# Performance work log

Hardware: AMD Instinct MI355X
Metric: run time of the kernel (lower is better)

The kernel has to match this reference:

```python
import jax, jax.numpy as jnp
import numpy as np
from math import sqrt

D_MODEL = 1024
N_HEADS = 16
D_KEYS = 64
D_LLM = 4096
B, L, N = 8, 512, 1000


def _init_params(key):
    ks = jax.random.split(key, 20)
    s = 0.02
    def lin(k, din, dout):
        return jax.random.normal(k, (din, dout), jnp.float32) * s
    p = {}
    for i, pre in enumerate(('t', 'd')):
        o = i * 8
        p[pre + '_Wq'] = lin(ks[o + 0], D_MODEL, N_HEADS * D_KEYS)
        p[pre + '_bq'] = jnp.zeros((N_HEADS * D_KEYS,), jnp.float32)
        p[pre + '_Wk'] = lin(ks[o + 1], D_LLM, N_HEADS * D_KEYS)
        p[pre + '_bk'] = jnp.zeros((N_HEADS * D_KEYS,), jnp.float32)
        p[pre + '_Wv'] = lin(ks[o + 2], D_LLM, N_HEADS * D_KEYS)
        p[pre + '_bv'] = jnp.zeros((N_HEADS * D_KEYS,), jnp.float32)
        p[pre + '_Wo'] = lin(ks[o + 3], N_HEADS * D_KEYS, D_LLM)
        p[pre + '_bo'] = jnp.zeros((D_LLM,), jnp.float32)
    # adaptive fusion gate MLP: Linear(2d->d), ReLU, Linear(d->1), Sigmoid
    p['g_W1'] = jax.random.normal(ks[16], (2 * D_MODEL, D_MODEL), jnp.float32) * sqrt(2.0 / (2 * D_MODEL))
    p['g_b1'] = jnp.zeros((D_MODEL,), jnp.float32)
    p['g_W2'] = jax.random.normal(ks[17], (D_MODEL, 1), jnp.float32) * s
    p['g_b2'] = jnp.zeros((1,), jnp.float32)  # gate_bias_init = 0.0
    return p


def setup_inputs() -> dict:
    key = jax.random.key(0)
    k1, k2, k3, k4, kp = jax.random.split(key, 5)
    inp = {
        'trend_embedding': jax.random.normal(k1, (B, L, D_MODEL), jnp.float32),
        'detail_embedding': jax.random.normal(k2, (B, L, D_MODEL), jnp.float32),
        'trend_prototypes': jax.random.normal(k3, (N, D_LLM), jnp.float32),
        'detail_prototypes': jax.random.normal(k4, (N, D_LLM), jnp.float32),
    }
    inp.update(_init_params(kp))
    return inp


def _reprogram(x, protos, Wq, bq, Wk, bk, Wv, bv, Wo, bo):
    # x: (B,L,d_model), protos: (S,d_llm)
    b, l, _ = x.shape
    s = protos.shape[0]
    q = (x @ Wq + bq).reshape(b, l, N_HEADS, D_KEYS)
    k = (protos @ Wk + bk).reshape(s, N_HEADS, D_KEYS)
    v = (protos @ Wv + bv).reshape(s, N_HEADS, D_KEYS)
    scale = 1.0 / sqrt(D_KEYS)
    scores = jnp.einsum('blhe,she->bhls', q, k)  # (B,H,L,S)
    A = jax.nn.softmax(scale * scores, axis=-1)  # dropout is eval-mode identity
    out = jnp.einsum('bhls,she->blhe', A, v).reshape(b, l, N_HEADS * D_KEYS)
    return out @ Wo + bo  # (B,L,d_llm)


def reference(trend_embedding, detail_embedding, trend_prototypes, detail_prototypes,
              t_Wq, t_bq, t_Wk, t_bk, t_Wv, t_bv, t_Wo, t_bo,
              d_Wq, d_bq, d_Wk, d_bk, d_Wv, d_bv, d_Wo, d_bo,
              g_W1, g_b1, g_W2, g_b2):
    sem_trend = _reprogram(trend_embedding, trend_prototypes,
                           t_Wq, t_bq, t_Wk, t_bk, t_Wv, t_bv, t_Wo, t_bo)
    sem_detail = _reprogram(detail_embedding, detail_prototypes,
                            d_Wq, d_bq, d_Wk, d_bk, d_Wv, d_bv, d_Wo, d_bo)
    # adaptive gate from raw embeddings
    combined = jnp.concatenate([trend_embedding, detail_embedding], axis=-1)
    h = jax.nn.relu(combined @ g_W1 + g_b1)
    gate = jax.nn.sigmoid(h @ g_W2 + g_b2)  # (B,L,1)
    return gate * sem_trend + (1.0 - gate) * sem_detail
```

## Files before the change

kernel.cpp:

```cpp
#include <hip/hip_runtime.h>

typedef unsigned short u16;
typedef unsigned int u32;
typedef __attribute__((ext_vector_type(4))) u16 u16x4;
typedef __attribute__((ext_vector_type(8))) u16 u16x8;
typedef __attribute__((ext_vector_type(4))) float f32x4;
typedef __attribute__((ext_vector_type(8))) __bf16 bf16x8;

#define DEV static __device__ __forceinline__

DEV u16 f2bf(float f) {
    u32 u = __builtin_bit_cast(u32, f);
    return (u16)((u + 0x7FFFu + ((u >> 16) & 1u)) >> 16);
}
DEV float bf2f(u16 h) { return __builtin_bit_cast(float, (u32)h << 16); }

DEV f32x4 mfma16(u16x8 a, u16x8 b, f32x4 c) {
    return __builtin_amdgcn_mfma_f32_16x16x32_bf16(
        __builtin_bit_cast(bf16x8, a), __builtin_bit_cast(bf16x8, b), c, 0, 0, 0);
}

DEV void gload16(const void* g, void* l) {
    __builtin_amdgcn_global_load_lds(
        (const __attribute__((address_space(1))) void*)g,
        (__attribute__((address_space(3))) void*)l, 16, 0, 0);
}


__global__ __launch_bounds__(256) void k_build_xcomb(
    const float* __restrict__ tr, const float* __restrict__ de, u16* __restrict__ out) {
    int i = blockIdx.x * 256 + threadIdx.x;
    int m = i >> 9;
    int c = (i & 511) * 4;
    const float* src = (c < 1024) ? (tr + (size_t)m * 1024 + c)
                                  : (de + (size_t)m * 1024 + (c - 1024));
    f32x4 v = *(const f32x4*)src;
    u16x4 o = { f2bf(v[0]), f2bf(v[1]), f2bf(v[2]), f2bf(v[3]) };
    *(u16x4*)(out + (size_t)m * 2048 + c) = o;
}

__global__ __launch_bounds__(256) void k_convert(
    const float* __restrict__ in, u16* __restrict__ out, int n4) {
    int i = blockIdx.x * 256 + threadIdx.x;
    if (i >= n4) return;
    f32x4 v = ((const f32x4*)in)[i];
    u16x4 o = { f2bf(v[0]), f2bf(v[1]), f2bf(v[2]), f2bf(v[3]) };
    ((u16x4*)out)[i] = o;
}


__global__ void k_transpose_f2b(const float* __restrict__ in, u16* __restrict__ out,
                                int R, int C, int ldo) {
    __shared__ float t[32][33];
    int c0 = blockIdx.x * 32, r0 = blockIdx.y * 32;
    int tx = threadIdx.x, ty = threadIdx.y;
#pragma unroll
    for (int j = 0; j < 4; j++)
        t[ty + j * 8][tx] = in[(size_t)(r0 + ty + j * 8) * C + c0 + tx];
    __syncthreads();
#pragma unroll
    for (int j = 0; j < 4; j++)
        out[(size_t)(c0 + ty + j * 8) * ldo + r0 + tx] = f2bf(t[tx][ty + j * 8]);
}

__global__ void k_transpose_b2b(const u16* __restrict__ in, int ldi,
                                u16* __restrict__ out, int ldo, int R, int C) {
    __shared__ u16 t[32][33];
    int c0 = blockIdx.x * 32, r0 = blockIdx.y * 32;
    int tx = threadIdx.x, ty = threadIdx.y;
#pragma unroll
    for (int j = 0; j < 4; j++)
        t[ty + j * 8][tx] = in[(size_t)(r0 + ty + j * 8) * ldi + c0 + tx];
    __syncthreads();
#pragma unroll
    for (int j = 0; j < 4; j++)
        out[(size_t)(c0 + ty + j * 8) * ldo + r0 + tx] = t[tx][ty + j * 8];
}

#define MODE_BF16 0
#define MODE_BF16_RELU 1
#define MODE_F32_GATED 2

__global__ __launch_bounds__(256) void k_gemm128(
    const u16* __restrict__ A0, const u16* __restrict__ A1, int lda,
    const u16* __restrict__ B0, const u16* __restrict__ B1, int K,
    void* __restrict__ o0, void* __restrict__ o1, int ldc, int mode,
    const float* __restrict__ b1_0, const float* __restrict__ b1_1,
    const float* __restrict__ b2_0, const float* __restrict__ b2_1,
    const float* __restrict__ gate) {
    __shared__ u16 As[128 * 32];
    __shared__ u16 Bs[128 * 32];
    const int z = blockIdx.z;
    const u16* A = z ? A1 : A0;
    const u16* Bt = z ? B1 : B0;
    void* outp = z ? o1 : o0;
    const float* bias1 = z ? b1_1 : b1_0;
    const float* bias2 = z ? b2_1 : b2_0;

    const int tid = threadIdx.x, lane = tid & 63, wid = tid >> 6;
    const int l16 = lane & 15, l4 = lane >> 4;
    const int n0 = blockIdx.x * 128, m0 = blockIdx.y * 128;
    const int wm = (wid >> 1) * 64, wn = (wid & 1) * 64;

    const int srow = wid * 32 + (lane >> 2);
    const int scol = (lane & 3) * 8;
    const u16* gA = A + (size_t)(m0 + srow) * lda + scol;
    const u16* gB = Bt + (size_t)(n0 + srow) * (size_t)K + scol;
    u16* lA = As + wid * 32 * 32;
    u16* lB = Bs + wid * 32 * 32;

    f32x4 acc[4][4] = {};

    for (int k0 = 0; k0 < K; k0 += 32) {
        gload16(gA, lA);
        gload16(gA + (size_t)16 * lda, lA + 16 * 32);
        gload16(gB, lB);
        gload16(gB + (size_t)16 * K, lB + 16 * 32);
        gA += 32;
        gB += 32;
        __syncthreads();
        u16x8 af[4], bfr[4];
#pragma unroll
        for (int m = 0; m < 4; m++) af[m] = *(const u16x8*)&As[(wm + m * 16 + l16) * 32 + l4 * 8];
#pragma unroll
        for (int n = 0; n < 4; n++) bfr[n] = *(const u16x8*)&Bs[(wn + n * 16 + l16) * 32 + l4 * 8];
#pragma unroll
        for (int m = 0; m < 4; m++)
#pragma unroll
            for (int n = 0; n < 4; n++)
                acc[m][n] = mfma16(af[m], bfr[n], acc[m][n]);
        __syncthreads();
    }

#pragma unroll
    for (int m = 0; m < 4; m++) {
#pragma unroll
        for (int n = 0; n < 4; n++) {
            int col = n0 + wn + n * 16 + l16;
#pragma unroll
            for (int j = 0; j < 4; j++) {
                int row = m0 + wm + m * 16 + l4 * 4 + j;
                float v = acc[m][n][j];
                if (mode == MODE_F32_GATED) {
                    float g = gate[row];
                    ((float*)outp)[(size_t)row * ldc + col] =
                        v + g * bias1[col] + (1.f - g) * bias2[col];
                } else {
                    float bb = (bias2 != nullptr && col >= 1024) ? bias2[col - 1024]
                                                                 : bias1[col];
                    v += bb;
                    if (mode == MODE_BF16_RELU) v = fmaxf(v, 0.f);
                    ((u16*)outp)[(size_t)row * ldc + col] = f2bf(v);
                }
            }
        }
    }
}

__global__ __launch_bounds__(256) void k_gate(const u16* __restrict__ h,
                                              const float* __restrict__ W2,
                                              const float* __restrict__ b2,
                                              float* __restrict__ gate) {
    int row = blockIdx.x * 4 + (threadIdx.x >> 6);
    int lane = threadIdx.x & 63;
    const u16* hp = h + (size_t)row * 1024 + lane * 16;
    u16x8 a = *(const u16x8*)hp;
    u16x8 b = *(const u16x8*)(hp + 8);
    const f32x4* wp = (const f32x4*)(W2 + lane * 16);
    f32x4 w0 = wp[0], w1 = wp[1], w2 = wp[2], w3 = wp[3];
    float s = 0.f;
#pragma unroll
    for (int i = 0; i < 4; i++) {
        s += bf2f(a[i]) * w0[i];
        s += bf2f(a[4 + i]) * w1[i];
        s += bf2f(b[i]) * w2[i];
        s += bf2f(b[4 + i]) * w3[i];
    }
#pragma unroll
    for (int d = 1; d < 64; d <<= 1) s += __shfl_xor(s, d);
    if (lane == 0) gate[row] = 1.f / (1.f + __expf(-(s + b2[0])));
}

__global__ __launch_bounds__(256) void k_attn(
    const u16* __restrict__ Q,
    const u16* __restrict__ Kb, int ldk,
    const u16* __restrict__ Vt,
    const float* __restrict__ gate, int isTrend,
    u16* __restrict__ outp, int ocol) {
    __shared__ u16 Ks[64][72];
    __shared__ u16 Vs[64][72];
    __shared__ u16 Ps[4][32][72];
    const int tid = threadIdx.x, lane = tid & 63, wid = tid >> 6;
    const int l16 = lane & 15, l4 = lane >> 4;
    const int qt = blockIdx.x, bh = blockIdx.y;
    const int b = bh >> 4, h = bh & 15;
    const int row0 = b * 512 + qt * 128 + wid * 32;

    u16x8 qf[2][2];
#pragma unroll
    for (int m = 0; m < 2; m++)
#pragma unroll
        for (int kc = 0; kc < 2; kc++)
            qf[m][kc] = *(const u16x8*)(Q + (size_t)(row0 + m * 16 + l16) * 1024 +
                                        h * 64 + kc * 32 + l4 * 8);

    float runm[2][4], runl[2][4];
#pragma unroll
    for (int m = 0; m < 2; m++)
#pragma unroll
        for (int j = 0; j < 4; j++) { runm[m][j] = -3.0e38f; runl[m][j] = 0.f; }
    f32x4 oacc[2][4] = {};

    for (int st = 0; st < 16; st++) {
        const int s0 = st * 64;
#pragma unroll
        for (int i = 0; i < 2; i++) {
            int idx = tid + i * 256;
            int rr = idx >> 3, cc = (idx & 7) * 8;
            *(u16x8*)&Ks[rr][cc] = *(const u16x8*)(Kb + (size_t)(s0 + rr) * ldk + h * 64 + cc);
            *(u16x8*)&Vs[rr][cc] = *(const u16x8*)(Vt + (size_t)(h * 64 + rr) * 1024 + s0 + cc);
        }
        __syncthreads();

        f32x4 sa[2][4] = {};
#pragma unroll
        for (int n = 0; n < 4; n++) {
#pragma unroll
            for (int kc = 0; kc < 2; kc++) {
                u16x8 kf = *(const u16x8*)&Ks[n * 16 + l16][kc * 32 + l4 * 8];
#pragma unroll
                for (int m = 0; m < 2; m++) sa[m][n] = mfma16(qf[m][kc], kf, sa[m][n]);
            }
        }
#pragma unroll
        for (int m = 0; m < 2; m++)
#pragma unroll
            for (int n = 0; n < 4; n++) {
                bool valid = (s0 + n * 16 + l16) < 1000;
#pragma unroll
                for (int j = 0; j < 4; j++)
                    sa[m][n][j] = valid ? sa[m][n][j] * 0.125f : -3.0e38f;
            }
#pragma unroll
        for (int m = 0; m < 2; m++) {
#pragma unroll
            for (int j = 0; j < 4; j++) {
                float rm = fmaxf(fmaxf(sa[m][0][j], sa[m][1][j]),
                                 fmaxf(sa[m][2][j], sa[m][3][j]));
#pragma unroll
                for (int d = 1; d < 16; d <<= 1) rm = fmaxf(rm, __shfl_xor(rm, d));
                float nm = fmaxf(runm[m][j], rm);
                float corr = __expf(runm[m][j] - nm);
                runm[m][j] = nm;
                float rs = 0.f;
#pragma unroll
                for (int n = 0; n < 4; n++) {
                    float p = __expf(sa[m][n][j] - nm);
                    sa[m][n][j] = p;
                    rs += p;
                }
#pragma unroll
                for (int d = 1; d < 16; d <<= 1) rs += __shfl_xor(rs, d);
                runl[m][j] = runl[m][j] * corr + rs;
#pragma unroll
                for (int n = 0; n < 4; n++) oacc[m][n][j] *= corr;
            }
        }
#pragma unroll
        for (int m = 0; m < 2; m++)
#pragma unroll
            for (int n = 0; n < 4; n++)
#pragma unroll
                for (int j = 0; j < 4; j++)
                    Ps[wid][m * 16 + l4 * 4 + j][n * 16 + l16] = f2bf(sa[m][n][j]);

        u16x8 pf[2][2];
#pragma unroll
        for (int m = 0; m < 2; m++)
#pragma unroll
            for (int kc = 0; kc < 2; kc++)
                pf[m][kc] = *(const u16x8*)&Ps[wid][m * 16 + l16][kc * 32 + l4 * 8];
#pragma unroll
        for (int ne = 0; ne < 4; ne++) {
#pragma unroll
            for (int kc = 0; kc < 2; kc++) {
                u16x8 vfr = *(const u16x8*)&Vs[ne * 16 + l16][kc * 32 + l4 * 8];
#pragma unroll
                for (int m = 0; m < 2; m++)
                    oacc[m][ne] = mfma16(pf[m][kc], vfr, oacc[m][ne]);
            }
        }
        __syncthreads();
    }

#pragma unroll
    for (int m = 0; m < 2; m++) {
#pragma unroll
        for (int j = 0; j < 4; j++) {
            int grow = row0 + m * 16 + l4 * 4 + j;
            float g = gate[grow];
            float wgt = isTrend ? g : (1.f - g);
            float f = wgt / runl[m][j];
#pragma unroll
            for (int ne = 0; ne < 4; ne++)
                outp[(size_t)grow * 2048 + ocol + h * 64 + ne * 16 + l16] =
                    f2bf(oacc[m][ne][j] * f);
        }
    }
}


extern "C" void kernel_launch(void* const* d_in, const int* in_sizes, int n_in,
                              void* d_out, int out_size, void* d_ws, size_t ws_size,
                              hipStream_t stream) {
    (void)in_sizes; (void)n_in; (void)out_size; (void)ws_size;
    const float* trend  = (const float*)d_in[0];
    const float* detail = (const float*)d_in[1];
    const float* tproto = (const float*)d_in[2];
    const float* dproto = (const float*)d_in[3];
    const float* t_Wq = (const float*)d_in[4];
    const float* t_bq = (const float*)d_in[5];
    const float* t_Wk = (const float*)d_in[6];
    const float* t_bk = (const float*)d_in[7];
    const float* t_Wv = (const float*)d_in[8];
    const float* t_bv = (const float*)d_in[9];
    const float* t_Wo = (const float*)d_in[10];
    const float* t_bo = (const float*)d_in[11];
    const float* d_Wq = (const float*)d_in[12];
    const float* d_bq = (const float*)d_in[13];
    const float* d_Wk = (const float*)d_in[14];
    const float* d_bk = (const float*)d_in[15];
    const float* d_Wv = (const float*)d_in[16];
    const float* d_bv = (const float*)d_in[17];
    const float* d_Wo = (const float*)d_in[18];
    const float* d_bo = (const float*)d_in[19];
    const float* g_W1 = (const float*)d_in[20];
    const float* g_b1 = (const float*)d_in[21];
    const float* g_W2 = (const float*)d_in[22];
    const float* g_b2 = (const float*)d_in[23];

    char* w = (char*)d_ws;
    auto alloc = [&](size_t bytes) {
        char* p = w;
        w += (bytes + 255) & ~(size_t)255;
        return p;
    };
    u16* xcomb  = (u16*)alloc(4096ull * 2048 * 2);
    u16* pt     = (u16*)alloc(1024ull * 4096 * 2);
    u16* pd     = (u16*)alloc(1024ull * 4096 * 2);
    u16* WqTt   = (u16*)alloc(1024ull * 1024 * 2);
    u16* WqTd   = (u16*)alloc(1024ull * 1024 * 2);
    u16* WkvTt  = (u16*)alloc(2048ull * 4096 * 2);
    u16* WkvTd  = (u16*)alloc(2048ull * 4096 * 2);
    u16* WoT    = (u16*)alloc(4096ull * 2048 * 2);
    u16* W1T    = (u16*)alloc(1024ull * 2048 * 2);
    u16* Qt     = (u16*)alloc(4096ull * 1024 * 2);
    u16* Qd     = (u16*)alloc(4096ull * 1024 * 2);
    u16* KVt    = (u16*)alloc(1024ull * 2048 * 2);
    u16* KVd    = (u16*)alloc(1024ull * 2048 * 2);
    u16* VtT    = (u16*)alloc(1024ull * 1024 * 2);
    u16* VdT    = (u16*)alloc(1024ull * 1024 * 2);
    u16* hbuf   = (u16*)alloc(4096ull * 1024 * 2);
    float* gateb = (float*)alloc(4096ull * 4);
    u16* attnc  = (u16*)alloc(4096ull * 2048 * 2);

    dim3 tb(32, 8);

    k_build_xcomb<<<8192, 256, 0, stream>>>(trend, detail, xcomb);
    k_convert<<<4000, 256, 0, stream>>>(tproto, pt, 1024000);
    k_convert<<<4000, 256, 0, stream>>>(dproto, pd, 1024000);
    hipMemsetAsync(pt + 1000ull * 4096, 0, 24ull * 4096 * 2, stream);
    hipMemsetAsync(pd + 1000ull * 4096, 0, 24ull * 4096 * 2, stream);

    k_transpose_f2b<<<dim3(32, 32), tb, 0, stream>>>(t_Wq, WqTt, 1024, 1024, 1024);
    k_transpose_f2b<<<dim3(32, 32), tb, 0, stream>>>(d_Wq, WqTd, 1024, 1024, 1024);
    k_transpose_f2b<<<dim3(32, 128), tb, 0, stream>>>(t_Wk, WkvTt, 4096, 1024, 4096);
    k_transpose_f2b<<<dim3(32, 128), tb, 0, stream>>>(t_Wv, WkvTt + 1024ull * 4096, 4096, 1024, 4096);
    k_transpose_f2b<<<dim3(32, 128), tb, 0, stream>>>(d_Wk, WkvTd, 4096, 1024, 4096);
    k_transpose_f2b<<<dim3(32, 128), tb, 0, stream>>>(d_Wv, WkvTd + 1024ull * 4096, 4096, 1024, 4096);
    k_transpose_f2b<<<dim3(128, 32), tb, 0, stream>>>(t_Wo, WoT, 1024, 4096, 2048);
    k_transpose_f2b<<<dim3(128, 32), tb, 0, stream>>>(d_Wo, WoT + 1024, 1024, 4096, 2048);
    k_transpose_f2b<<<dim3(32, 64), tb, 0, stream>>>(g_W1, W1T, 2048, 1024, 2048);

    k_gemm128<<<dim3(8, 32, 1), 256, 0, stream>>>(
        xcomb, nullptr, 2048, W1T, nullptr, 2048, hbuf, nullptr, 1024,
        MODE_BF16_RELU, g_b1, nullptr, nullptr, nullptr, nullptr);
    k_gate<<<1024, 256, 0, stream>>>(hbuf, g_W2, g_b2, gateb);

    k_gemm128<<<dim3(8, 32, 2), 256, 0, stream>>>(
        xcomb, xcomb + 1024, 2048, WqTt, WqTd, 1024, Qt, Qd, 1024,
        MODE_BF16, t_bq, d_bq, nullptr, nullptr, nullptr);

    k_gemm128<<<dim3(16, 8, 2), 256, 0, stream>>>(
        pt, pd, 4096, WkvTt, WkvTd, 4096, KVt, KVd, 2048,
        MODE_BF16, t_bk, d_bk, t_bv, d_bv, nullptr);

    k_transpose_b2b<<<dim3(32, 32), tb, 0, stream>>>(KVt + 1024, 2048, VtT, 1024, 1024, 1024);
    k_transpose_b2b<<<dim3(32, 32), tb, 0, stream>>>(KVd + 1024, 2048, VdT, 1024, 1024, 1024);

    k_attn<<<dim3(4, 128), 256, 0, stream>>>(Qt, KVt, 2048, VtT, gateb, 1, attnc, 0);
    k_attn<<<dim3(4, 128), 256, 0, stream>>>(Qd, KVd, 2048, VdT, gateb, 0, attnc, 1024);

    k_gemm128<<<dim3(32, 32, 1), 256, 0, stream>>>(
        attnc, nullptr, 2048, WoT, nullptr, 2048, (float*)d_out, nullptr, 4096,
        MODE_F32_GATED, t_bo, nullptr, d_bo, nullptr, gateb);
}
```

Measured before the change: 752.5 us.

## Add 256x256 pipelined gated output GEMM and merge GEMM and attention launches

Adds a new 512-thread GEMM for the large gated output projection. It uses 256x256 tiles, XOR-swizzled LDS, double-buffered asynchronous global-to-LDS loads interleaved with MFMA phases, and setprio scheduling, replacing the 128x128 kernel for that step. The gate-MLP GEMM and both Q projections now share one launch through a per-z argument struct, and the two attention launches are merged into one grid along z. The aim is better operand reuse and load/compute overlap in the biggest GEMM, plus fewer launches and fuller grids. In exchange it uses 128KB of LDS per block and adds more complex wait-count logic.

After: 647.0 us. 1.16x faster.

```diff
diff --git a/kernel.cpp b/kernel.cpp
--- a/kernel.cpp
+++ b/kernel.cpp
@@ -79,23 +79,29 @@
 
 #define MODE_BF16 0
 #define MODE_BF16_RELU 1
-#define MODE_F32_GATED 2
-
-__global__ __launch_bounds__(256) void k_gemm128(
-    const u16* __restrict__ A0, const u16* __restrict__ A1, int lda,
-    const u16* __restrict__ B0, const u16* __restrict__ B1, int K,
-    void* __restrict__ o0, void* __restrict__ o1, int ldc, int mode,
-    const float* __restrict__ b1_0, const float* __restrict__ b1_1,
-    const float* __restrict__ b2_0, const float* __restrict__ b2_1,
-    const float* __restrict__ gate) {
+
+struct GemmArgs {
+    const u16* A[3];
+    const u16* B[3];
+    u16* o[3];
+    const float* bias1[3];
+    const float* bias2[3];
+    int K[3];
+    int lda[3];
+    int ldc[3];
+    int mode[3];
+};
+
+__global__ __launch_bounds__(256) void k_gemm128(GemmArgs ga) {
     __shared__ u16 As[128 * 32];
     __shared__ u16 Bs[128 * 32];
     const int z = blockIdx.z;
-    const u16* A = z ? A1 : A0;
-    const u16* Bt = z ? B1 : B0;
-    void* outp = z ? o1 : o0;
-    const float* bias1 = z ? b1_1 : b1_0;
-    const float* bias2 = z ? b2_1 : b2_0;
+    const u16* A = ga.A[z];
+    const u16* Bt = ga.B[z];
+    u16* outp = ga.o[z];
+    const float* bias1 = ga.bias1[z];
+    const float* bias2 = ga.bias2[z];
+    const int K = ga.K[z], lda = ga.lda[z], ldc = ga.ldc[z], mode = ga.mode[z];
 
     const int tid = threadIdx.x, lane = tid & 63, wid = tid >> 6;
     const int l16 = lane & 15, l4 = lane >> 4;
@@ -141,17 +147,129 @@
             for (int j = 0; j < 4; j++) {
                 int row = m0 + wm + m * 16 + l4 * 4 + j;
                 float v = acc[m][n][j];
-                if (mode == MODE_F32_GATED) {
-                    float g = gate[row];
-                    ((float*)outp)[(size_t)row * ldc + col] =
-                        v + g * bias1[col] + (1.f - g) * bias2[col];
-                } else {
-                    float bb = (bias2 != nullptr && col >= 1024) ? bias2[col - 1024]
-                                                                 : bias1[col];
-                    v += bb;
-                    if (mode == MODE_BF16_RELU) v = fmaxf(v, 0.f);
-                    ((u16*)outp)[(size_t)row * ldc + col] = f2bf(v);
-                }
+                float bb = (bias2 != nullptr && col >= 1024) ? bias2[col - 1024] : bias1[col];
+                v += bb;
+                if (mode == MODE_BF16_RELU) v = fmaxf(v, 0.f);
+                outp[(size_t)row * ldc + col] = f2bf(v);
+            }
+        }
+    }
+}
+
+__global__ __launch_bounds__(512, 2) void k_gemm256g(
+    const u16* __restrict__ A, int ldaE,
+    const u16* __restrict__ Bt, int ldbE,
+    int K,
+    float* __restrict__ C, int ldcE,
+    const float* __restrict__ bias1, const float* __restrict__ bias2,
+    const float* __restrict__ gate) {
+    __shared__ __attribute__((aligned(16))) u16 sm[2 * 32768];
+    char* smc = (char*)sm;
+
+    const int tid = threadIdx.x, lane = tid & 63, wid = tid >> 6;
+    const int l16 = lane & 15, l4 = lane >> 4;
+    const int wm = (wid >> 2) * 128;
+    const int wn = (wid & 3) * 64;
+    const int m0 = blockIdx.y * 256, n0 = blockIdx.x * 256;
+
+    const int p0 = wid * 1024 + lane * 16;
+    const int p1 = p0 + 8192;
+    const int rr0 = p0 >> 7, rr1 = p1 >> 7;
+    const int cb0 = (p0 & 127) ^ ((rr0 & 7) << 4);
+    const int cb1 = (p1 & 127) ^ ((rr1 & 7) << 4);
+    const size_t ldaB = (size_t)ldaE * 2, ldbB = (size_t)ldbE * 2;
+    const char* Ab = (const char*)A;
+    const char* Bb = (const char*)Bt;
+    const size_t aOff0 = (size_t)(m0 + rr0) * ldaB + cb0;
+    const size_t aOff1 = (size_t)(m0 + rr1) * ldaB + cb1;
+    const size_t bOff0 = (size_t)(n0 + rr0) * ldbB + cb0;
+    const size_t bOff1 = (size_t)(n0 + rr1) * ldbB + cb1;
+
+    auto stageA = [&](int T, int h) {
+        size_t tOff = (size_t)T * 128 + (size_t)h * 128 * ldaB;
+        char* d = smc + (T & 1) * 65536 + h * 16384 + wid * 1024;
+        gload16(Ab + aOff0 + tOff, d);
+        gload16(Ab + aOff1 + tOff, d + 8192);
+    };
+    auto stageB = [&](int T, int h) {
+        size_t tOff = (size_t)T * 128 + (size_t)h * 128 * ldbB;
+        char* d = smc + (T & 1) * 65536 + 32768 + h * 16384 + wid * 1024;
+        gload16(Bb + bOff0 + tOff, d);
+        gload16(Bb + bOff1 + tOff, d + 8192);
+    };
+    auto readA = [&](int buf, int mf, int kc) -> u16x8 {
+        int row = wm + mf * 16 + l16;
+        int cb = (kc * 64 + l4 * 16) ^ ((l16 & 7) << 4);
+        return *(const u16x8*)(smc + buf * 65536 + row * 128 + cb);
+    };
+    auto readB = [&](int buf, int nf, int kc) -> u16x8 {
+        int row = wn + nf * 16 + l16;
+        int cb = (kc * 64 + l4 * 16) ^ ((l16 & 7) << 4);
+        return *(const u16x8*)(smc + buf * 65536 + 32768 + row * 128 + cb);
+    };
+
+    f32x4 acc[8][4] = {};
+    const int NT = K >> 6;
+
+    stageA(0, 0); stageA(0, 1);
+    stageB(0, 0); stageB(0, 1);
+    stageB(1, 0); stageB(1, 1);
+    asm volatile("s_waitcnt vmcnt(4)" ::: "memory");
+    __builtin_amdgcn_s_barrier();
+
+    for (int t = 0; t < NT; ++t) {
+        const int buf = t & 1;
+        u16x8 bfr[4][2];
+#pragma unroll
+        for (int q = 0; q < 4; ++q) {
+            u16x8 af[2][2];
+            if (q == 0) {
+#pragma unroll
+                for (int nf = 0; nf < 4; nf++)
+#pragma unroll
+                    for (int kc = 0; kc < 2; kc++) bfr[nf][kc] = readB(buf, nf, kc);
+            }
+#pragma unroll
+            for (int im = 0; im < 2; im++)
+#pragma unroll
+                for (int kc = 0; kc < 2; kc++) af[im][kc] = readA(buf, 2 * q + im, kc);
+
+            if (q == 0) { if (t + 1 < NT) stageA(t + 1, 0); }
+            else if (q == 1) { if (t + 1 < NT) stageA(t + 1, 1); }
+            else if (q == 2) { if (t + 2 < NT) stageB(t + 2, 0); }
+            else { if (t + 2 < NT) stageB(t + 2, 1); }
+
+            asm volatile("" ::: "memory");
+            __builtin_amdgcn_s_barrier();
+            __builtin_amdgcn_s_setprio(1);
+#pragma unroll
+            for (int im = 0; im < 2; im++)
+#pragma unroll
+                for (int nf = 0; nf < 4; nf++)
+#pragma unroll
+                    for (int kc = 0; kc < 2; kc++)
+                        acc[2 * q + im][nf] = mfma16(af[im][kc], bfr[nf][kc], acc[2 * q + im][nf]);
+            __builtin_amdgcn_s_setprio(0);
+            asm volatile("" ::: "memory");
+            if (q == 3) {
+                if (t + 2 < NT) asm volatile("s_waitcnt vmcnt(4)" ::: "memory");
+                else            asm volatile("s_waitcnt vmcnt(0)" ::: "memory");
+            }
+            __builtin_amdgcn_s_barrier();
+        }
+    }
+
+#pragma unroll
+    for (int mf = 0; mf < 8; mf++) {
+#pragma unroll
+        for (int j = 0; j < 4; j++) {
+            int row = m0 + wm + mf * 16 + l4 * 4 + j;
+            float g = gate[row];
+#pragma unroll
+            for (int nf = 0; nf < 4; nf++) {
+                int col = n0 + wn + nf * 16 + l16;
+                C[(size_t)row * ldcE + col] =
+                    acc[mf][nf][j] + g * bias1[col] + (1.f - g) * bias2[col];
             }
         }
     }
@@ -182,14 +300,21 @@
 }
 
 __global__ __launch_bounds__(256) void k_attn(
-    const u16* __restrict__ Q,
-    const u16* __restrict__ Kb, int ldk,
-    const u16* __restrict__ Vt,
-    const float* __restrict__ gate, int isTrend,
-    u16* __restrict__ outp, int ocol) {
+    const u16* __restrict__ Q0, const u16* __restrict__ Q1,
+    const u16* __restrict__ KV0, const u16* __restrict__ KV1, int ldk,
+    const u16* __restrict__ Vt0, const u16* __restrict__ Vt1,
+    const float* __restrict__ gate,
+    u16* __restrict__ outp) {
     __shared__ u16 Ks[64][72];
     __shared__ u16 Vs[64][72];
     __shared__ u16 Ps[4][32][72];
+    const int z = blockIdx.z;
+    const u16* Q = z ? Q1 : Q0;
+    const u16* Kb = z ? KV1 : KV0;
+    const u16* Vt = z ? Vt1 : Vt0;
+    const int isTrend = (z == 0);
+    const int ocol = z * 1024;
+
     const int tid = threadIdx.x, lane = tid & 63, wid = tid >> 6;
     const int l16 = lane & 15, l4 = lane >> 4;
     const int qt = blockIdx.x, bh = blockIdx.y;
@@ -382,26 +507,38 @@
     k_transpose_f2b<<<dim3(128, 32), tb, 0, stream>>>(d_Wo, WoT + 1024, 1024, 4096, 2048);
     k_transpose_f2b<<<dim3(32, 64), tb, 0, stream>>>(g_W1, W1T, 2048, 1024, 2048);
 
-    k_gemm128<<<dim3(8, 32, 1), 256, 0, stream>>>(
-        xcomb, nullptr, 2048, W1T, nullptr, 2048, hbuf, nullptr, 1024,
-        MODE_BF16_RELU, g_b1, nullptr, nullptr, nullptr, nullptr);
+    {
+        GemmArgs ga = {};
+        ga.A[0] = xcomb;        ga.B[0] = W1T;  ga.o[0] = hbuf;
+        ga.bias1[0] = g_b1;     ga.K[0] = 2048; ga.lda[0] = 2048; ga.ldc[0] = 1024;
+        ga.mode[0] = MODE_BF16_RELU;
+        ga.A[1] = xcomb;        ga.B[1] = WqTt; ga.o[1] = Qt;
+        ga.bias1[1] = t_bq;     ga.K[1] = 1024; ga.lda[1] = 2048; ga.ldc[1] = 1024;
+        ga.mode[1] = MODE_BF16;
+        ga.A[2] = xcomb + 1024; ga.B[2] = WqTd; ga.o[2] = Qd;
+        ga.bias1[2] = d_bq;     ga.K[2] = 1024; ga.lda[2] = 2048; ga.ldc[2] = 1024;
+        ga.mode[2] = MODE_BF16;
+        k_gemm128<<<dim3(8, 32, 3), 256, 0, stream>>>(ga);
+    }
     k_gate<<<1024, 256, 0, stream>>>(hbuf, g_W2, g_b2, gateb);
 
-    k_gemm128<<<dim3(8, 32, 2), 256, 0, stream>>>(
-        xcomb, xcomb + 1024, 2048, WqTt, WqTd, 1024, Qt, Qd, 1024,
-        MODE_BF16, t_bq, d_bq, nullptr, nullptr, nullptr);
-
-    k_gemm128<<<dim3(16, 8, 2), 256, 0, stream>>>(
-        pt, pd, 4096, WkvTt, WkvTd, 4096, KVt, KVd, 2048,
-        MODE_BF16, t_bk, d_bk, t_bv, d_bv, nullptr);
+    {
+        GemmArgs ga = {};
+        ga.A[0] = pt; ga.B[0] = WkvTt; ga.o[0] = KVt;
+        ga.bias1[0] = t_bk; ga.bias2[0] = t_bv;
+        ga.K[0] = 4096; ga.lda[0] = 4096; ga.ldc[0] = 2048; ga.mode[0] = MODE_BF16;
+        ga.A[1] = pd; ga.B[1] = WkvTd; ga.o[1] = KVd;
+        ga.bias1[1] = d_bk; ga.bias2[1] = d_bv;
+        ga.K[1] = 4096; ga.lda[1] = 4096; ga.ldc[1] = 2048; ga.mode[1] = MODE_BF16;
+        k_gemm128<<<dim3(16, 8, 2), 256, 0, stream>>>(ga);
+    }
 
     k_transpose_b2b<<<dim3(32, 32), tb, 0, stream>>>(KVt + 1024, 2048, VtT, 1024, 1024, 1024);
     k_transpose_b2b<<<dim3(32, 32), tb, 0, stream>>>(KVd + 1024, 2048, VdT, 1024, 1024, 1024);
 
-    k_attn<<<dim3(4, 128), 256, 0, stream>>>(Qt, KVt, 2048, VtT, gateb, 1, attnc, 0);
-    k_attn<<<dim3(4, 128), 256, 0, stream>>>(Qd, KVd, 2048, VdT, gateb, 0, attnc, 1024);
-
-    k_gemm128<<<dim3(32, 32, 1), 256, 0, stream>>>(
-        attnc, nullptr, 2048, WoT, nullptr, 2048, (float*)d_out, nullptr, 4096,
-        MODE_F32_GATED, t_bo, nullptr, d_bo, nullptr, gateb);
-}
+    k_attn<<<dim3(4, 128, 2), 256, 0, stream>>>(Qt, Qd, KVt, KVd, 2048, VtT, VdT,
+                                                gateb, attnc);
+
+    k_gemm256g<<<dim3(16, 16), 512, 0, stream>>>(attnc, 2048, WoT, 2048, 2048,
+                                                 (float*)d_out, 4096, t_bo, d_bo, gateb);
+}
```
